# Performance work log

Measured on AMD Instinct MI355X. Metric: run time of the kernel, lower is better.

The kernel has to match this reference:

```python
import math
import jax, jax.numpy as jnp
from jax import lax
import numpy as np

NHEADS = 8
GN_GROUPS = 32
GN_EPS = 1e-5
L2_EPS = 1e-12


def conv2d(x, w, b=None, groups=1):
    # x: [B,C,H,W], w: [O, I/groups, kh, kw], stride 1, torch padding=k//2 (SAME)
    out = lax.conv_general_dilated(
        x, w, window_strides=(1, 1), padding='SAME',
        dimension_numbers=('NCHW', 'OIHW', 'NCHW'),
        feature_group_count=groups)
    if b is not None:
        out = out + b[None, :, None, None]
    return out


def group_norm(x, scale, bias, groups, eps=GN_EPS):
    B, C, H, W = x.shape
    xg = x.reshape(B, groups, C // groups, H, W)
    mu = jnp.mean(xg, axis=(2, 3, 4), keepdims=True)
    var = jnp.var(xg, axis=(2, 3, 4), keepdims=True)
    xg = (xg - mu) * lax.rsqrt(var + eps)
    x = xg.reshape(B, C, H, W)
    return x * scale[None, :, None, None] + bias[None, :, None, None]


def l2norm_ch(x):
    # F.normalize(x, dim=1): divide by channel L2 norm, clamped at eps
    n = jnp.sqrt(jnp.sum(x * x, axis=1, keepdims=True))
    return x / jnp.maximum(n, L2_EPS)


def attn_op(q, k, v, nheads, scale):
    # q,k,v: [B, C, xf, yf] real; tokens = frequency bins, features = C/nheads
    b, c, xf, yf = q.shape
    hd = c // nheads
    qh = q.reshape(b, nheads, hd, xf * yf)
    kh = k.reshape(b, nheads, hd, xf * yf)
    vh = v.reshape(b, nheads, hd, xf * yf)
    sim = jnp.einsum('bhcm,bhcn->bhmn', qh, kh) * scale
    attn = jax.nn.softmax(sim, axis=-1)
    out = jnp.einsum('bhmn,bhcn->bhcm', attn, vh)
    return out.reshape(b, c, xf, yf)


def setup_inputs() -> dict:
    key = jax.random.key(0)
    ks = jax.random.split(key, 14)
    B, H, W = 4, 48, 48
    fea = cond_c = qkv = dout = 256

    def rn(k, shape, s=0.05):
        return jax.random.normal(k, shape, dtype=jnp.float32) * s

    return {
        'x': jax.random.normal(ks[0], (B, fea, H, W), jnp.float32),
        'cond': jax.random.normal(ks[1], (B, cond_c, H, W), jnp.float32),
        'gn_w': jnp.ones((fea,), jnp.float32),
        'gn_b': jnp.zeros((fea,), jnp.float32),
        'q_dw': rn(ks[2], (fea, 1, 3, 3)),          # depthwise 3x3, groups=fea
        'q_pw_w': rn(ks[3], (qkv, fea, 1, 1)),
        'q_pw_b': jnp.zeros((qkv,), jnp.float32),
        'kv_dw': rn(ks[4], (cond_c, 1, 3, 3)),
        'kv_pw_w': rn(ks[5], (2 * qkv, cond_c, 1, 1)),
        'kv_pw_b': jnp.zeros((2 * qkv,), jnp.float32),
        'attn_out_w': rn(ks[6], (dout, qkv, 1, 1)),
        'attn_out_b': jnp.zeros((dout,), jnp.float32),
        'ffn_w1': rn(ks[7], (2 * dout, dout, 3, 3)),
        'ffn_w2': rn(ks[8], (dout, 2 * dout, 3, 3)),
        'ffn_w3': rn(ks[9], (dout, dout, 1, 1)),
        'ffn_b3': jnp.zeros((dout,), jnp.float32),
    }


def reference(x, cond, gn_w, gn_b, q_dw, q_pw_w, q_pw_b, kv_dw, kv_pw_w, kv_pw_b,
              attn_out_w, attn_out_b, ffn_w1, ffn_w2, ffn_w3, ffn_b3):
    B, C, H, W = x.shape
    qkv_dim = q_pw_w.shape[0]
    scale = 1.0 / math.sqrt(qkv_dim // NHEADS)

    xn = group_norm(x, gn_w, gn_b, GN_GROUPS)
    q = conv2d(conv2d(xn, q_dw, groups=C), q_pw_w, q_pw_b)
    kv = conv2d(conv2d(cond, kv_dw, groups=cond.shape[1]), kv_pw_w, kv_pw_b)
    k, v = jnp.split(kv, 2, axis=1)
    q, k, v = l2norm_ch(q), l2norm_ch(k), l2norm_ch(v)

    qf = jnp.fft.rfft2(q, axes=(-2, -1), norm='ortho')
    kf = jnp.fft.rfft2(k, axes=(-2, -1), norm='ortho')
    vf = jnp.fft.rfft2(v, axes=(-2, -1), norm='ortho')

    amp = attn_op(jnp.abs(qf), jnp.abs(kf), jnp.abs(vf), NHEADS, scale)
    phas = attn_op(jnp.angle(qf), jnp.angle(kf), jnp.angle(vf), NHEADS, scale)
    outc = lax.complex(amp * jnp.cos(phas), amp * jnp.sin(phas))  # torch.polar
    out = jnp.fft.irfft2(outc, s=(H, W), axes=(-2, -1), norm='ortho')

    attn_out = conv2d(out, attn_out_w, attn_out_b) + xn  # attn_res = Identity (fea_dim == dim_out)
    h1 = jax.nn.silu(conv2d(attn_out, ffn_w1))
    h2 = conv2d(h1, ffn_w2)
    ffn = conv2d(h2, ffn_w3, ffn_b3)
    # DropPath is identity in eval mode
    return ffn + attn_out
```

## Files before the change

### kernel.cpp

```cpp
#include <hip/hip_runtime.h>
#include <hip/hip_bf16.h>
#include <math.h>

constexpr int Bn = 4, Cn = 256, Hn = 48, Wn = 48, HW = 2304;
constexpr float ATT_SCALE = 0.17677669529663687f;

typedef __attribute__((ext_vector_type(8))) short bf16x8;
typedef __attribute__((ext_vector_type(4))) float f32x4;

#define MFMA16(A, B, C) __builtin_amdgcn_mfma_f32_16x16x32_bf16(A, B, C, 0, 0, 0)

__global__ void gn1_kernel(const float* __restrict__ x, float* __restrict__ part) {
  int bg = blockIdx.x >> 2, ck = blockIdx.x & 3;
  const float4* xp = (const float4*)(x + (size_t)bg * 18432 + ck * 4608);
  float s = 0.f, ss = 0.f;
  for (int i = threadIdx.x; i < 1152; i += 256) {
    float4 v = xp[i];
    s += v.x + v.y + v.z + v.w;
    ss += v.x * v.x + v.y * v.y + v.z * v.z + v.w * v.w;
  }
#pragma unroll
  for (int off = 32; off; off >>= 1) { s += __shfl_xor(s, off); ss += __shfl_xor(ss, off); }
  __shared__ float rs[4], rss[4];
  int wid = threadIdx.x >> 6;
  if ((threadIdx.x & 63) == 0) { rs[wid] = s; rss[wid] = ss; }
  __syncthreads();
  if (threadIdx.x == 0) {
    part[blockIdx.x * 2] = rs[0] + rs[1] + rs[2] + rs[3];
    part[blockIdx.x * 2 + 1] = rss[0] + rss[1] + rss[2] + rss[3];
  }
}

__global__ void gn2_kernel(const float* __restrict__ x, const float* __restrict__ part,
                           const float* __restrict__ gw, const float* __restrict__ gb,
                           float* __restrict__ y) {
  int bg = blockIdx.x >> 2, ck = blockIdx.x & 3;
  float s = part[bg * 8] + part[bg * 8 + 2] + part[bg * 8 + 4] + part[bg * 8 + 6];
  float ss = part[bg * 8 + 1] + part[bg * 8 + 3] + part[bg * 8 + 5] + part[bg * 8 + 7];
  float mean = s * (1.f / 18432.f);
  float var = ss * (1.f / 18432.f) - mean * mean;
  float inv = rsqrtf(var + 1e-5f);
  int g = bg & 31;
  const float4* xp = (const float4*)(x + (size_t)bg * 18432 + ck * 4608);
  float4* yp = (float4*)(y + (size_t)bg * 18432 + ck * 4608);
  for (int i = threadIdx.x; i < 1152; i += 256) {
    int c = (g << 3) + ((ck * 1152 + i) / 576);
    float w = gw[c] * inv, b = gb[c];
    float4 v = xp[i];
    v.x = (v.x - mean) * w + b; v.y = (v.y - mean) * w + b;
    v.z = (v.z - mean) * w + b; v.w = (v.w - mean) * w + b;
    yp[i] = v;
  }
}

__global__ void dw3x3_kernel(const float* __restrict__ in, const float* __restrict__ wd,
                             __hip_bfloat16* __restrict__ oh, __hip_bfloat16* __restrict__ ol) {
  int bc = blockIdx.x;
  int c = bc & 255;
  const float* ip = in + (size_t)bc * HW;
  const size_t ob = ((size_t)((bc >> 8) * 8 + (c >> 5)) * HW) * 32 + (c & 31);
  float w[9];
#pragma unroll
  for (int k = 0; k < 9; ++k) w[k] = wd[c * 9 + k];
  for (int p = threadIdx.x; p < HW; p += 256) {
    int yy = p / 48, xx = p - yy * 48;
    float a = 0.f;
#pragma unroll
    for (int ky = 0; ky < 3; ++ky) {
      int y2 = yy + ky - 1;
      if ((unsigned)y2 < 48u) {
#pragma unroll
        for (int kx = 0; kx < 3; ++kx) {
          int x2 = xx + kx - 1;
          if ((unsigned)x2 < 48u) a += ip[y2 * 48 + x2] * w[ky * 3 + kx];
        }
      }
    }
    __hip_bfloat16 h = __float2bfloat16(a);
    oh[ob + (size_t)p * 32] = h;
    ol[ob + (size_t)p * 32] = __float2bfloat16(a - __bfloat162float(h));
  }
}

__global__ void pwpack_kernel(const float* __restrict__ w, __hip_bfloat16* __restrict__ WH,
                              __hip_bfloat16* __restrict__ WL, int O) {
  int q = blockIdx.x * 256 + threadIdx.x;
  int o = q >> 8, c = q & 255;
  float v = w[q];
  __hip_bfloat16 h = __float2bfloat16(v);
  size_t idx = ((size_t)(c >> 5) * O + o) * 32 + (c & 31);
  WH[idx] = h;
  WL[idx] = __float2bfloat16(v - __bfloat162float(h));
}

template <bool RES>
__global__ void __launch_bounds__(256)
pw5_kernel(const __hip_bfloat16* __restrict__ XH, const __hip_bfloat16* __restrict__ XL,
           const __hip_bfloat16* __restrict__ WH, const __hip_bfloat16* __restrict__ WL,
           const float* __restrict__ bias, const float* __restrict__ res, size_t res_bs,
           float* __restrict__ out, size_t out_bs, int CO) {
  const int tid = threadIdx.x;
  const int wv = tid >> 6, lane = tid & 63, lm = lane & 15, kg = lane >> 4;
  const int px0 = blockIdx.x * 128;
  const int ob = blockIdx.y * 64;
  const int img = blockIdx.z;

  f32x4 acc[4][2];
#pragma unroll
  for (int mt = 0; mt < 4; ++mt) {
    acc[mt][0] = (f32x4){0.f, 0.f, 0.f, 0.f};
    acc[mt][1] = (f32x4){0.f, 0.f, 0.f, 0.f};
  }

  const size_t bb = (size_t)img * 589824 + (size_t)(px0 + wv * 32 + lm) * 32 + kg * 8;
#pragma unroll
  for (int ci = 0; ci < 8; ++ci) {
    const size_t bo = bb + (size_t)ci * 73728;
    bf16x8 BH0 = *(const bf16x8*)(XH + bo);
    bf16x8 BH1 = *(const bf16x8*)(XH + bo + 512);
    bf16x8 BL0 = *(const bf16x8*)(XL + bo);
    bf16x8 BL1 = *(const bf16x8*)(XL + bo + 512);
    const size_t wb = ((size_t)ci * CO + ob + lm) * 32 + kg * 8;
#pragma unroll
    for (int mt = 0; mt < 4; ++mt) {
      bf16x8 AH = *(const bf16x8*)(WH + wb + mt * 512);
      bf16x8 AL = *(const bf16x8*)(WL + wb + mt * 512);
      acc[mt][0] = MFMA16(AH, BH0, acc[mt][0]);
      acc[mt][0] = MFMA16(AH, BL0, acc[mt][0]);
      acc[mt][0] = MFMA16(AL, BH0, acc[mt][0]);
      acc[mt][1] = MFMA16(AH, BH1, acc[mt][1]);
      acc[mt][1] = MFMA16(AH, BL1, acc[mt][1]);
      acc[mt][1] = MFMA16(AL, BH1, acc[mt][1]);
    }
  }

#pragma unroll
  for (int mt = 0; mt < 4; ++mt) {
#pragma unroll
    for (int g = 0; g < 2; ++g) {
      int px = px0 + wv * 32 + g * 16 + lm;
#pragma unroll
      for (int r = 0; r < 4; ++r) {
        int o = ob + mt * 16 + kg * 4 + r;
        float v = acc[mt][g][r] + bias[o];
        if (RES) v += res[(size_t)img * res_bs + (size_t)o * HW + px];
        out[(size_t)img * out_bs + (size_t)o * HW + px] = v;
      }
    }
  }
}

__global__ void l2n_kernel(float* __restrict__ t, size_t bstride) {
  int pxl = threadIdx.x & 63;
  int cg = threadIdx.x >> 6;
  int p = blockIdx.x * 64 + pxl;
  float* q = t + (size_t)blockIdx.y * bstride + p;
  float ss = 0.f;
#pragma unroll 8
  for (int c = cg * 64; c < cg * 64 + 64; ++c) { float v = q[(size_t)c * HW]; ss += v * v; }
  __shared__ float part[4][64];
  __shared__ float sinv[64];
  part[cg][pxl] = ss;
  __syncthreads();
  if (threadIdx.x < 64) {
    float tot = part[0][pxl] + part[1][pxl] + part[2][pxl] + part[3][pxl];
    sinv[pxl] = 1.f / fmaxf(sqrtf(tot), 1e-12f);
  }
  __syncthreads();
  float inv = sinv[pxl];
#pragma unroll 8
  for (int c = cg * 64; c < cg * 64 + 64; ++c) q[(size_t)c * HW] *= inv;
}

__global__ void dftmat_kernel(__hip_bfloat16* __restrict__ mt) {
  int t = blockIdx.x * 256 + threadIdx.x;
  const float TP = 6.283185307179586f;
  if (t < 4096) {
    int up = t >> 6, w = t & 63;
    float v = 0.f;
    if (w < 48 && up < 50) {
      int u = (up < 25) ? up : up - 25;
      float ang = TP * (float)((w * u) % 48) / 48.f;
      v = ((up < 25) ? cosf(ang) : -sinf(ang)) * (1.f / 48.f);
    }
    __hip_bfloat16 h = __float2bfloat16(v);
    mt[t] = h; mt[4096 + t] = __float2bfloat16(v - __bfloat162float(h));
  } else if (t < 7168) {
    int q = t - 4096;
    int vv = q >> 6, h = q & 63;
    float c = 0.f, s = 0.f;
    if (h < 48) {
      float ang = TP * (float)((vv * h) % 48) / 48.f;
      c = cosf(ang); s = sinf(ang);
    }
    __hip_bfloat16 ch = __float2bfloat16(c);
    mt[8192 + q] = ch; mt[11264 + q] = __float2bfloat16(c - __bfloat162float(ch));
    __hip_bfloat16 sh = __float2bfloat16(s);
    mt[14336 + q] = sh; mt[17408 + q] = __float2bfloat16(s - __bfloat162float(sh));
  } else if (t < 8704) {
    int q = t - 7168;
    int w = q >> 5, u = q & 31;
    float c = 0.f, s = 0.f;
    if (u < 25) {
      float ang = TP * (float)((u * w) % 48) / 48.f;
      c = cosf(ang); s = -sinf(ang);
    }
    __hip_bfloat16 ch = __float2bfloat16(c);
    mt[20480 + q] = ch; mt[22016 + q] = __float2bfloat16(c - __bfloat162float(ch));
    __hip_bfloat16 sh = __float2bfloat16(s);
    mt[23552 + q] = sh; mt[25088 + q] = __float2bfloat16(s - __bfloat162float(sh));
  }
}

template <bool TLAY>
__global__ void __launch_bounds__(256)
rfft2_mfma(const float* __restrict__ in, size_t bstride, const __hip_bfloat16* __restrict__ mt,
           __hip_bfloat16* __restrict__ amp, __hip_bfloat16* __restrict__ pha) {
  const int bc = blockIdx.x;
  const int bi = bc >> 8, ch = bc & 255;
  const float* ip = in + (size_t)bi * bstride + (size_t)ch * HW;
  __shared__ __align__(16) __hip_bfloat16 XH[48 * 72], XL[48 * 72];
  __shared__ __align__(16) __hip_bfloat16 Yt[4][32 * 72];
  const int tid = threadIdx.x;
  const int lane = tid & 63, lm = lane & 15, kg = lane >> 4, wv = tid >> 6;

  for (int i = tid; i < 48 * 72; i += 256) {
    int r = i / 72, w = i - r * 72;
    float v = (w < 48) ? ip[r * 48 + w] : 0.f;
    __hip_bfloat16 h = __float2bfloat16(v);
    XH[i] = h;
    XL[i] = __float2bfloat16(v - __bfloat162float(h));
  }
  for (int i = tid; i < 4 * 32 * 72; i += 256) ((unsigned short*)Yt)[i] = 0;
  __syncthreads();

  {
    const __hip_bfloat16* W1TH = mt;
    const __hip_bfloat16* W1TL = mt + 4096;
    const int brow = wv * 16 + lm;
    bf16x8 BH0 = *(const bf16x8*)(W1TH + brow * 64 + kg * 8);
    bf16x8 BH1 = *(const bf16x8*)(W1TH + brow * 64 + 32 + kg * 8);
    bf16x8 BL0 = *(const bf16x8*)(W1TL + brow * 64 + kg * 8);
    bf16x8 BL1 = *(const bf16x8*)(W1TL + brow * 64 + 32 + kg * 8);
#pragma unroll
    for (int mtI = 0; mtI < 3; ++mtI) {
      f32x4 acc = {0.f, 0.f, 0.f, 0.f};
      bf16x8 AH = *(const bf16x8*)(&XH[(mtI * 16 + lm) * 72 + kg * 8]);
      bf16x8 AL = *(const bf16x8*)(&XL[(mtI * 16 + lm) * 72 + kg * 8]);
      acc = MFMA16(AH, BH0, acc); acc = MFMA16(AH, BL0, acc); acc = MFMA16(AL, BH0, acc);
      AH = *(const bf16x8*)(&XH[(mtI * 16 + lm) * 72 + 32 + kg * 8]);
      AL = *(const bf16x8*)(&XL[(mtI * 16 + lm) * 72 + 32 + kg * 8]);
      acc = MFMA16(AH, BH1, acc); acc = MFMA16(AH, BL1, acc); acc = MFMA16(AL, BH1, acc);
      if (brow < 50) {
        int aidx = (brow < 25) ? 0 : 2;
        int u = (brow < 25) ? brow : brow - 25;
#pragma unroll
        for (int r = 0; r < 4; ++r) {
          int h = mtI * 16 + kg * 4 + r;
          float v = acc[r];
          __hip_bfloat16 hh = __float2bfloat16(v);
          Yt[aidx][u * 72 + h] = hh;
          Yt[aidx + 1][u * 72 + h] = __float2bfloat16(v - __bfloat162float(hh));
        }
      }
    }
  }
  __syncthreads();

  {
    const __hip_bfloat16* M2CH = mt + 8192;
    const __hip_bfloat16* M2CL = mt + 11264;
    const __hip_bfloat16* M2SH = mt + 14336;
    const __hip_bfloat16* M2SL = mt + 17408;
    for (int t = wv; t < 6; t += 4) {
      int mtI = t >> 1, ntI = t & 1;
      f32x4 aC1 = {0.f,0.f,0.f,0.f}, aS1 = {0.f,0.f,0.f,0.f};
      f32x4 aC2 = {0.f,0.f,0.f,0.f}, aS2 = {0.f,0.f,0.f,0.f};
#pragma unroll
      for (int ks = 0; ks < 2; ++ks) {
        int arow = mtI * 16 + lm;
        int k0 = ks * 32 + kg * 8;
        bf16x8 CH = *(const bf16x8*)(M2CH + arow * 64 + k0);
        bf16x8 CL = *(const bf16x8*)(M2CL + arow * 64 + k0);
        bf16x8 SH = *(const bf16x8*)(M2SH + arow * 64 + k0);
        bf16x8 SL = *(const bf16x8*)(M2SL + arow * 64 + k0);
        int brow = ntI * 16 + lm;
        bf16x8 ReH = *(const bf16x8*)(&Yt[0][brow * 72 + k0]);
        bf16x8 ReL = *(const bf16x8*)(&Yt[1][brow * 72 + k0]);
        bf16x8 ImH = *(const bf16x8*)(&Yt[2][brow * 72 + k0]);
        bf16x8 ImL = *(const bf16x8*)(&Yt[3][brow * 72 + k0]);
        aC1 = MFMA16(CH, ReH, aC1); aC1 = MFMA16(CH, ReL, aC1); aC1 = MFMA16(CL, ReH, aC1);
        aS2 = MFMA16(SH, ImH, aS2); aS2 = MFMA16(SH, ImL, aS2); aS2 = MFMA16(SL, ImH, aS2);
        aC2 = MFMA16(CH, ImH, aC2); aC2 = MFMA16(CH, ImL, aC2); aC2 = MFMA16(CL, ImH, aC2);
        aS1 = MFMA16(SH, ReH, aS1); aS1 = MFMA16(SH, ReL, aS1); aS1 = MFMA16(SL, ReH, aS1);
      }
      int u = ntI * 16 + lm;
      if (u < 25) {
#pragma unroll
        for (int r = 0; r < 4; ++r) {
          int v = mtI * 16 + kg * 4 + r;
          float zre = aC1[r] + aS2[r];
          float zim = aC2[r] - aS1[r];
          float am = sqrtf(zre * zre + zim * zim);
          float ph = atan2f(zim, zre);
          int i = v * 25 + u;
          size_t o;
          if (TLAY) o = ((size_t)(bc >> 5) * 1200 + i) * 32 + (bc & 31);
          else      o = (size_t)bc * 1200 + i;
          amp[o] = __float2bfloat16(am);
          pha[o] = __float2bfloat16(ph);
        }
      }
    }
  }
}

__global__ void __launch_bounds__(256)
polar_irfft2_mfma(const float* __restrict__ amp, const float* __restrict__ pha,
                  const __hip_bfloat16* __restrict__ mt,
                  __hip_bfloat16* __restrict__ oh, __hip_bfloat16* __restrict__ ol) {
  const int bc = blockIdx.x;
  __shared__ __align__(16) __hip_bfloat16 Zt[4][32 * 72];
  __shared__ __align__(16) __hip_bfloat16 Yp[4][48 * 56];
  const int tid = threadIdx.x;
  const int lane = tid & 63, lm = lane & 15, kg = lane >> 4, wv = tid >> 6;

  for (int i = tid; i < 4 * 32 * 72; i += 256) ((unsigned short*)Zt)[i] = 0;
  for (int i = tid; i < 4 * 48 * 56; i += 256) ((unsigned short*)Yp)[i] = 0;
  __syncthreads();
  for (int i = tid; i < 1200; i += 256) {
    int v = i / 25, u = i - v * 25;
    float a = amp[(size_t)bc * 1200 + i];
    float p = pha[(size_t)bc * 1200 + i];
    float sc = (u == 0 || u == 24) ? (1.f / 48.f) : (2.f / 48.f);
    float zre = a * cosf(p) * sc;
    float zim = a * sinf(p) * sc;
    __hip_bfloat16 h0 = __float2bfloat16(zre);
    Zt[0][u * 72 + v] = h0;
    Zt[1][u * 72 + v] = __float2bfloat16(zre - __bfloat162float(h0));
    __hip_bfloat16 h1 = __float2bfloat16(zim);
    Zt[2][u * 72 + v] = h1;
    Zt[3][u * 72 + v] = __float2bfloat16(zim - __bfloat162float(h1));
  }
  __syncthreads();

  {
    const __hip_bfloat16* M2CH = mt + 8192;
    const __hip_bfloat16* M2CL = mt + 11264;
    const __hip_bfloat16* M2SH = mt + 14336;
    const __hip_bfloat16* M2SL = mt + 17408;
    for (int t = wv; t < 6; t += 4) {
      int mtI = t >> 1, ntI = t & 1;
      f32x4 aC1 = {0.f,0.f,0.f,0.f}, aS1 = {0.f,0.f,0.f,0.f};
      f32x4 aC2 = {0.f,0.f,0.f,0.f}, aS2 = {0.f,0.f,0.f,0.f};
#pragma unroll
      for (int ks = 0; ks < 2; ++ks) {
        int arow = mtI * 16 + lm;
        int k0 = ks * 32 + kg * 8;
        bf16x8 CH = *(const bf16x8*)(M2CH + arow * 64 + k0);
        bf16x8 CL = *(const bf16x8*)(M2CL + arow * 64 + k0);
        bf16x8 SH = *(const bf16x8*)(M2SH + arow * 64 + k0);
        bf16x8 SL = *(const bf16x8*)(M2SL + arow * 64 + k0);
        int brow = ntI * 16 + lm;
        bf16x8 ReH = *(const bf16x8*)(&Zt[0][brow * 72 + k0]);
        bf16x8 ReL = *(const bf16x8*)(&Zt[1][brow * 72 + k0]);
        bf16x8 ImH = *(const bf16x8*)(&Zt[2][brow * 72 + k0]);
        bf16x8 ImL = *(const bf16x8*)(&Zt[3][brow * 72 + k0]);
        aC1 = MFMA16(CH, ReH, aC1); aC1 = MFMA16(CH, ReL, aC1); aC1 = MFMA16(CL, ReH, aC1);
        aS2 = MFMA16(SH, ImH, aS2); aS2 = MFMA16(SH, ImL, aS2); aS2 = MFMA16(SL, ImH, aS2);
        aC2 = MFMA16(CH, ImH, aC2); aC2 = MFMA16(CH, ImL, aC2); aC2 = MFMA16(CL, ImH, aC2);
        aS1 = MFMA16(SH, ReH, aS1); aS1 = MFMA16(SH, ReL, aS1); aS1 = MFMA16(SL, ReH, aS1);
      }
      int u = ntI * 16 + lm;
      if (u < 25) {
#pragma unroll
        for (int r = 0; r < 4; ++r) {
          int h = mtI * 16 + kg * 4 + r;
          float yre = aC1[r] - aS2[r];
          float yim = aS1[r] + aC2[r];
          __hip_bfloat16 h0 = __float2bfloat16(yre);
          Yp[0][h * 56 + u] = h0;
          Yp[1][h * 56 + u] = __float2bfloat16(yre - __bfloat162float(h0));
          __hip_bfloat16 h1 = __float2bfloat16(yim);
          Yp[2][h * 56 + u] = h1;
          Yp[3][h * 56 + u] = __float2bfloat16(yim - __bfloat162float(h1));
        }
      }
    }
  }
  __syncthreads();

  {
    const __hip_bfloat16* W3CH = mt + 20480;
    const __hip_bfloat16* W3CL = mt + 22016;
    const __hip_bfloat16* W3SH = mt + 23552;
    const __hip_bfloat16* W3SL = mt + 25088;
    const int cch = bc & 255;
    const size_t obase = ((size_t)((bc >> 8) * 8 + (cch >> 5)) * HW) * 32 + (cch & 31);
    for (int t = wv; t < 9; t += 4) {
      int mtI = t / 3, ntI = t - (t / 3) * 3;
      f32x4 acc = {0.f, 0.f, 0.f, 0.f};
      int k0 = kg * 8;
      bf16x8 AH = *(const bf16x8*)(&Yp[0][(mtI * 16 + lm) * 56 + k0]);
      bf16x8 AL = *(const bf16x8*)(&Yp[1][(mtI * 16 + lm) * 56 + k0]);
      bf16x8 IH = *(const bf16x8*)(&Yp[2][(mtI * 16 + lm) * 56 + k0]);
      bf16x8 IL = *(const bf16x8*)(&Yp[3][(mtI * 16 + lm) * 56 + k0]);
      int brow = ntI * 16 + lm;
      bf16x8 CH = *(const bf16x8*)(W3CH + brow * 32 + k0);
      bf16x8 CL = *(const bf16x8*)(W3CL + brow * 32 + k0);
      bf16x8 SH = *(const bf16x8*)(W3SH + brow * 32 + k0);
      bf16x8 SL = *(const bf16x8*)(W3SL + brow * 32 + k0);
      acc = MFMA16(AH, CH, acc); acc = MFMA16(AH, CL, acc); acc = MFMA16(AL, CH, acc);
      acc = MFMA16(IH, SH, acc); acc = MFMA16(IH, SL, acc); acc = MFMA16(IL, SH, acc);
#pragma unroll
      for (int r = 0; r < 4; ++r) {
        int h = mtI * 16 + kg * 4 + r;
        int p = h * 48 + brow;
        float v = acc[r];
        __hip_bfloat16 hh = __float2bfloat16(v);
        oh[obase + (size_t)p * 32] = hh;
        ol[obase + (size_t)p * 32] = __float2bfloat16(v - __bfloat162float(hh));
      }
    }
  }
}

__global__ void __launch_bounds__(64)
attn_mfma2x(const __hip_bfloat16* __restrict__ Qb, const __hip_bfloat16* __restrict__ Kb,
            const __hip_bfloat16* __restrict__ Vb, float* __restrict__ Ob) {
  const int lin = blockIdx.x;
  const int xcd = lin & 7;
  const int idx = lin >> 3;
  const int pr = xcd * 8 + idx / 75;
  const int m0 = (idx % 75) * 16;
  const int z = pr >> 5;
  const int bh = pr & 31;
  const __hip_bfloat16* Qt = Qb + (size_t)z * 1228800;
  const __hip_bfloat16* Kt = Kb + (size_t)z * 1228800;
  const __hip_bfloat16* Vc = Vb + (size_t)z * 1228800;
  float* Om = Ob + (size_t)z * 1228800;
  const int lane = threadIdx.x;
  const int lm = lane & 15, kg = lane >> 4;
  __shared__ unsigned short Pl[16][40];
  __shared__ float fl[16];
  __shared__ float linv[16];
  const __hip_bfloat16* Qp = Qt + ((size_t)bh * 1200 + m0) * 32;
  const __hip_bfloat16* Kp = Kt + (size_t)bh * 38400;
  const __hip_bfloat16* Vp = Vc + (size_t)bh * 38400;
  const bf16x8 qf = *(const bf16x8*)(Qp + lm * 32 + kg * 8);
  const float Cs = ATT_SCALE * 1.44269504f;

  f32x4 acc0 = {0.f, 0.f, 0.f, 0.f}, acc1 = {0.f, 0.f, 0.f, 0.f};
  float psum = 0.f, mreg = -3.0e38f;

  for (int g = 0; g < 38; ++g) {
    const int n0 = g * 32;
    const bool t1ok = (g < 37);
    bf16x8 kf0 = *(const bf16x8*)(Kp + (size_t)(n0 + lm) * 32 + kg * 8);
    f32x4 d0 = {0.f, 0.f, 0.f, 0.f};
    d0 = MFMA16(kf0, qf, d0);
    f32x4 d1 = {0.f, 0.f, 0.f, 0.f};
    if (t1ok) {
      bf16x8 kf1 = *(const bf16x8*)(Kp + (size_t)(n0 + 16 + lm) * 32 + kg * 8);
      d1 = MFMA16(kf1, qf, d1);
    }
    float tm = fmaxf(fmaxf(d0[0], d0[1]), fmaxf(d0[2], d0[3]));
    if (t1ok) tm = fmaxf(tm, fmaxf(fmaxf(d1[0], d1[1]), fmaxf(d1[2], d1[3])));
    tm = fmaxf(tm, __shfl_xor(tm, 16));
    tm = fmaxf(tm, __shfl_xor(tm, 32));
    float nm = fmaxf(mreg, tm);
    float ff = exp2f((mreg - nm) * Cs);
    mreg = nm;
    if (kg == 0) fl[lm] = ff;
    const float mb = nm * Cs;
    float p0 = exp2f(d0[0] * Cs - mb), p1 = exp2f(d0[1] * Cs - mb);
    float p2 = exp2f(d0[2] * Cs - mb), p3 = exp2f(d0[3] * Cs - mb);
    float ps = p0 + p1 + p2 + p3;
    ushort4 pk0, pk1;
    pk0.x = __builtin_bit_cast(unsigned short, __float2bfloat16(p0));
    pk0.y = __builtin_bit_cast(unsigned short, __float2bfloat16(p1));
    pk0.z = __builtin_bit_cast(unsigned short, __float2bfloat16(p2));
    pk0.w = __builtin_bit_cast(unsigned short, __float2bfloat16(p3));
    if (t1ok) {
      float q0 = exp2f(d1[0] * Cs - mb), q1 = exp2f(d1[1] * Cs - mb);
      float q2 = exp2f(d1[2] * Cs - mb), q3 = exp2f(d1[3] * Cs - mb);
      ps += q0 + q1 + q2 + q3;
      pk1.x = __builtin_bit_cast(unsigned short, __float2bfloat16(q0));
      pk1.y = __builtin_bit_cast(unsigned short, __float2bfloat16(q1));
      pk1.z = __builtin_bit_cast(unsigned short, __float2bfloat16(q2));
      pk1.w = __builtin_bit_cast(unsigned short, __float2bfloat16(q3));
    } else {
      pk1.x = pk1.y = pk1.z = pk1.w = 0;
    }
    psum = psum * ff + ps;
    *(ushort4*)(&Pl[lm][kg * 4]) = pk0;
    *(ushort4*)(&Pl[lm][16 + kg * 4]) = pk1;
    float4 f4 = *(const float4*)(&fl[kg * 4]);
    acc0[0] *= f4.x; acc0[1] *= f4.y; acc0[2] *= f4.z; acc0[3] *= f4.w;
    acc1[0] *= f4.x; acc1[1] *= f4.y; acc1[2] *= f4.z; acc1[3] *= f4.w;
    bf16x8 pa = *(const bf16x8*)(&Pl[lm][kg * 8]);
    bf16x8 v0 = *(const bf16x8*)(Vp + (size_t)lm * 1200 + n0 + kg * 8);
    bf16x8 v1 = *(const bf16x8*)(Vp + (size_t)(16 + lm) * 1200 + n0 + kg * 8);
    acc0 = MFMA16(pa, v0, acc0);
    acc1 = MFMA16(pa, v1, acc1);
  }
  psum += __shfl_xor(psum, 16);
  psum += __shfl_xor(psum, 32);
  if (kg == 0) linv[lm] = 1.f / psum;
  __syncthreads();
#pragma unroll
  for (int r = 0; r < 4; ++r) {
    int m = m0 + kg * 4 + r;
    float li = linv[kg * 4 + r];
    Om[(size_t)bh * 38400 + (size_t)lm * 1200 + m] = acc0[r] * li;
    Om[(size_t)bh * 38400 + (size_t)(16 + lm) * 1200 + m] = acc1[r] * li;
  }
}

__global__ void packx_kernel(const float* __restrict__ in, __hip_bfloat16* __restrict__ xp) {
  int y = blockIdx.x;
  int b = blockIdx.y;
  int c = threadIdx.x;
  const float* ip = in + ((size_t)(b * 256 + c) * 48 + y) * 48;
  __hip_bfloat16* op = xp + ((size_t)(b * 8 + (c >> 5)) * 2500 + (size_t)(y + 1) * 50 + 1) * 32 + (c & 31);
  for (int x = 0; x < 48; ++x) op[x * 32] = __float2bfloat16(ip[x]);
}

template <int CIN>
__global__ void packw_kernel(const float* __restrict__ w, __hip_bfloat16* __restrict__ wp, int O) {
  int t = blockIdx.x * 256 + threadIdx.x;
  int o = t / CIN, c = t - o * CIN;
  if (o >= O) return;
  constexpr int NC = CIN / 32;
#pragma unroll
  for (int tap = 0; tap < 9; ++tap)
    wp[(((size_t)tap * NC + (c >> 5)) * O + o) * 32 + (c & 31)] = __float2bfloat16(w[(size_t)t * 9 + tap]);
}

__global__ void addpack_kernel(const float* __restrict__ a, const float* __restrict__ b,
                               __hip_bfloat16* __restrict__ oh, __hip_bfloat16* __restrict__ ol) {
  int i = blockIdx.x * 256 + threadIdx.x;
  float4 x = ((const float4*)a)[i];
  float4 y = ((const float4*)b)[i];
  x.x += y.x; x.y += y.y; x.z += y.z; x.w += y.w;
  int e = i * 4;
  int img = e / 589824, rem = e - img * 589824;
  int c = rem / 2304, px = rem - c * 2304;
  size_t ob = ((size_t)(img * 8 + (c >> 5)) * HW) * 32 + (c & 31);
  float vv[4] = {x.x, x.y, x.z, x.w};
#pragma unroll
  for (int j = 0; j < 4; ++j) {
    __hip_bfloat16 h = __float2bfloat16(vv[j]);
    oh[ob + (size_t)(px + j) * 32] = h;
    ol[ob + (size_t)(px + j) * 32] = __float2bfloat16(vv[j] - __bfloat162float(h));
  }
}

template <int CIN, int CO, bool TO_PAD, int KS>
__global__ void __launch_bounds__(256)
mfconv3x3(const __hip_bfloat16* __restrict__ Xp, const __hip_bfloat16* __restrict__ Wp,
          __hip_bfloat16* __restrict__ Op, float* __restrict__ Of) {
  constexpr int NC = CIN / 32;
  constexpr int KC = NC / KS;
  constexpr int MT = CO / 32;
  const int q = gridDim.x >> 3;
  const int swz = (blockIdx.x & 7) * q + (blockIdx.x >> 3);
  const int mt = swz % MT;
  const int ks = (swz / MT) % KS;
  const int rq = swz / (MT * KS);
  const int img = rq / 12;
  const int y0b = (rq % 12) * 4;
  const int tid = threadIdx.x;
  const int wv = tid >> 6;
  const int y = y0b + wv;
  const int lane = tid & 63;
  const int lm = lane & 15, kg = lane >> 4;
  const int o0 = mt * 32;
  const int ci0 = ks * KC;

  __shared__ __hip_bfloat16 Als[9216];
  __shared__ __hip_bfloat16 Bls[9600];

  f32x4 acc[2][3];
#pragma unroll
  for (int f = 0; f < 2; ++f)
#pragma unroll
    for (int g = 0; g < 3; ++g) acc[f][g] = (f32x4){0.f, 0.f, 0.f, 0.f};

  for (int ci = 0; ci < KC; ++ci) {
    const int cic = ci0 + ci;
    const size_t wst = ((size_t)cic * CO + o0) * 32;
    const size_t bst = ((size_t)(img * NC + cic) * 2500 + (size_t)y0b * 50) * 32;
    __syncthreads();
    for (int c = tid; c < 2352; c += 256) {
      if (c < 1152) {
        int tap = c >> 7, rem = c & 127;
        float4 v = *(const float4*)(Wp + wst + (size_t)tap * (NC * CO * 32) + rem * 8);
        *(float4*)(&Als[c * 8]) = v;
      } else {
        int c2 = c - 1152;
        float4 v = *(const float4*)(Xp + bst + (size_t)c2 * 8);
        *(float4*)(&Bls[c2 * 8]) = v;
      }
    }
    __syncthreads();
#pragma unroll
    for (int tap = 0; tap < 9; ++tap) {
      const int dy = tap / 3 - 1, dx = tap - (tap / 3) * 3 - 1;
      bf16x8 A0 = *(const bf16x8*)(&Als[tap * 1024 + lm * 32 + kg * 8]);
      bf16x8 A1 = *(const bf16x8*)(&Als[tap * 1024 + 512 + lm * 32 + kg * 8]);
      const int bbase = ((wv + 1 + dy) * 50 + 1 + dx + lm) * 32 + kg * 8;
      bf16x8 B0 = *(const bf16x8*)(&Bls[bbase]);
      bf16x8 B1 = *(const bf16x8*)(&Bls[bbase + 512]);
      bf16x8 B2 = *(const bf16x8*)(&Bls[bbase + 1024]);
      acc[0][0] = MFMA16(A0, B0, acc[0][0]);
      acc[0][1] = MFMA16(A0, B1, acc[0][1]);
      acc[0][2] = MFMA16(A0, B2, acc[0][2]);
      acc[1][0] = MFMA16(A1, B0, acc[1][0]);
      acc[1][1] = MFMA16(A1, B1, acc[1][1]);
      acc[1][2] = MFMA16(A1, B2, acc[1][2]);
    }
  }

  if (TO_PAD) {
    const int cio = o0 >> 5;
#pragma unroll
    for (int f = 0; f < 2; ++f) {
      const int cc = f * 16 + kg * 4;
#pragma unroll
      for (int g = 0; g < 3; ++g) {
        int x = g * 16 + lm;
        ushort4 st;
        float v0 = acc[f][g][0], v1 = acc[f][g][1], v2 = acc[f][g][2], v3 = acc[f][g][3];
        v0 = v0 / (1.f + __expf(-v0)); v1 = v1 / (1.f + __expf(-v1));
        v2 = v2 / (1.f + __expf(-v2)); v3 = v3 / (1.f + __expf(-v3));
        st.x = __builtin_bit_cast(unsigned short, __float2bfloat16(v0));
        st.y = __builtin_bit_cast(unsigned short, __float2bfloat16(v1));
        st.z = __builtin_bit_cast(unsigned short, __float2bfloat16(v2));
        st.w = __builtin_bit_cast(unsigned short, __float2bfloat16(v3));
        *(ushort4*)(Op + (((size_t)(img * (CO / 32) + cio) * 2500 + (size_t)(y + 1) * 50 + (x + 1)) * 32 + cc)) = st;
      }
    }
  } else {
    float* Ofp = Of + (size_t)ks * 4 * CO * HW;
#pragma unroll
    for (int f = 0; f < 2; ++f)
#pragma unroll
      for (int g = 0; g < 3; ++g) {
        int x = g * 16 + lm;
#pragma unroll
        for (int r = 0; r < 4; ++r) {
          int o = o0 + f * 16 + kg * 4 + r;
          Ofp[((size_t)img * CO + o) * HW + y * 48 + x] = acc[f][g][r];
        }
      }
  }
}

extern "C" void kernel_launch(void* const* d_in, const int* in_sizes, int n_in,
                              void* d_out, int out_size, void* d_ws, size_t ws_size,
                              hipStream_t stream) {
  (void)in_sizes; (void)n_in; (void)out_size; (void)ws_size;
  const float* x      = (const float*)d_in[0];
  const float* cond   = (const float*)d_in[1];
  const float* gn_w   = (const float*)d_in[2];
  const float* gn_b   = (const float*)d_in[3];
  const float* q_dw   = (const float*)d_in[4];
  const float* q_pw_w = (const float*)d_in[5];
  const float* q_pw_b = (const float*)d_in[6];
  const float* kv_dw  = (const float*)d_in[7];
  const float* kv_pw_w= (const float*)d_in[8];
  const float* kv_pw_b= (const float*)d_in[9];
  const float* ao_w   = (const float*)d_in[10];
  const float* ao_b   = (const float*)d_in[11];
  const float* w1     = (const float*)d_in[12];
  const float* w2     = (const float*)d_in[13];
  const float* w3     = (const float*)d_in[14];
  const float* b3     = (const float*)d_in[15];
  float* ws = (float*)d_ws;
  float* Yo = (float*)d_out;

  const size_t U = 2359296;
  const size_t Hf = 1228800;
  const size_t CS = 589824;
  const size_t CS2 = 1179648;

  float* XN  = ws;
  __hip_bfloat16* DWH = (__hip_bfloat16*)(ws + U);
  __hip_bfloat16* DWL = DWH + 2359296;
  float* Qb  = ws + 2 * U;
  float* KV  = ws + 3 * U;
  __hip_bfloat16* AQT = (__hip_bfloat16*)(ws + 5 * U);
  __hip_bfloat16* PQT = AQT + 1228800;
  __hip_bfloat16* AKT = AQT + 2 * 1228800;
  __hip_bfloat16* PKT = AQT + 3 * 1228800;
  __hip_bfloat16* AVc = AQT + 4 * 1228800;
  __hip_bfloat16* PVc = AQT + 5 * 1228800;
  float* AO  = ws + 5 * U + 3 * Hf;
  float* PO  = AO + Hf;
  __hip_bfloat16* OUTH = (__hip_bfloat16*)(ws + U);
  __hip_bfloat16* OUTL = OUTH + 2359296;
  float* ATT = ws + 5 * U;
  __hip_bfloat16* Xp1 = (__hip_bfloat16*)(ws + U);
  __hip_bfloat16* Xp2 = (__hip_bfloat16*)(ws + 2 * U);
  __hip_bfloat16* Wp1 = (__hip_bfloat16*)(ws + 2 * U + 2600000);
  __hip_bfloat16* Wp2 = (__hip_bfloat16*)(ws + 2 * U + 3200000);
  float* H2  = ws;
  float* H2b = ws + U;
  __hip_bfloat16* H2H = (__hip_bfloat16*)(ws + 5 * U + 3 * Hf);
  __hip_bfloat16* H2L = H2H + 2359296;
  __hip_bfloat16* BW = (__hip_bfloat16*)(ws + 5 * U + 5 * Hf);
  __hip_bfloat16* QWH = BW,            * QWL = BW + 65536;
  __hip_bfloat16* KWH = BW + 131072,   * KWL = BW + 262144;
  __hip_bfloat16* AWH = BW + 393216,   * AWL = BW + 458752;
  __hip_bfloat16* W3H = BW + 524288,   * W3L = BW + 589824;
  __hip_bfloat16* MT  = BW + 655360;
  float* GNP = ws + 5 * U + 5 * Hf + 341000;

  pwpack_kernel<<<256, 256, 0, stream>>>(q_pw_w, QWH, QWL, 256);
  pwpack_kernel<<<512, 256, 0, stream>>>(kv_pw_w, KWH, KWL, 512);
  pwpack_kernel<<<256, 256, 0, stream>>>(ao_w, AWH, AWL, 256);
  pwpack_kernel<<<256, 256, 0, stream>>>(w3, W3H, W3L, 256);
  dftmat_kernel<<<34, 256, 0, stream>>>(MT);
  gn1_kernel<<<512, 256, 0, stream>>>(x, GNP);
  gn2_kernel<<<512, 256, 0, stream>>>(x, GNP, gn_w, gn_b, XN);
  dw3x3_kernel<<<1024, 256, 0, stream>>>(XN, q_dw, DWH, DWL);
  pw5_kernel<false><<<dim3(18, 4, 4), 256, 0, stream>>>(DWH, DWL, QWH, QWL, q_pw_b, nullptr, 0, Qb, CS, 256);
  dw3x3_kernel<<<1024, 256, 0, stream>>>(cond, kv_dw, DWH, DWL);
  pw5_kernel<false><<<dim3(18, 8, 4), 256, 0, stream>>>(DWH, DWL, KWH, KWL, kv_pw_b, nullptr, 0, KV, CS2, 512);
  l2n_kernel<<<dim3(36, 4), 256, 0, stream>>>(Qb, CS);
  l2n_kernel<<<dim3(36, 4), 256, 0, stream>>>(KV, CS2);
  l2n_kernel<<<dim3(36, 4), 256, 0, stream>>>(KV + CS, CS2);
  rfft2_mfma<true ><<<1024, 256, 0, stream>>>(Qb, CS, MT, AQT, PQT);
  rfft2_mfma<true ><<<1024, 256, 0, stream>>>(KV, CS2, MT, AKT, PKT);
  rfft2_mfma<false><<<1024, 256, 0, stream>>>(KV + CS, CS2, MT, AVc, PVc);
  attn_mfma2x<<<4800, 64, 0, stream>>>(AQT, AKT, AVc, AO);
  polar_irfft2_mfma<<<1024, 256, 0, stream>>>(AO, PO, MT, OUTH, OUTL);
  pw5_kernel<true><<<dim3(18, 4, 4), 256, 0, stream>>>(OUTH, OUTL, AWH, AWL, ao_b, XN, CS, ATT, CS, 256);
  hipMemsetAsync(Xp1, 0, 2560000 * sizeof(__hip_bfloat16), stream);
  hipMemsetAsync(Xp2, 0, 5120000 * sizeof(__hip_bfloat16), stream);
  packx_kernel<<<dim3(48, 4), 256, 0, stream>>>(ATT, Xp1);
  packw_kernel<256><<<512, 256, 0, stream>>>(w1, Wp1, 512);
  packw_kernel<512><<<512, 256, 0, stream>>>(w2, Wp2, 256);
  mfconv3x3<256, 512, true, 1><<<768, 256, 0, stream>>>(Xp1, Wp1, Xp2, nullptr);
  mfconv3x3<512, 256, false, 2><<<768, 256, 0, stream>>>(Xp2, Wp2, nullptr, H2);
  addpack_kernel<<<2304, 256, 0, stream>>>(H2, H2b, H2H, H2L);
  pw5_kernel<true><<<dim3(18, 4, 4), 256, 0, stream>>>(H2H, H2L, W3H, W3L, b3, ATT, CS, Yo, CS, 256);
}
```

Before: 484.7 us.

## Widen attention key tiles, skip redundant rescales, register-prefetch conv input slabs

The frequency-domain attention kernel now processes 64 keys per iteration instead of 32. It also skips the online-softmax rescale of the accumulators and row sums when no row maximum grows, using a wave ballot to decide. The 3x3 conv kernel no longer stages weights in LDS; it reads them directly from global memory per tap. It also double-buffers the input slab through registers so the next channel chunk's load overlaps the current MFMAs. Together these cut loop overhead, exp and rescale work, and LDS traffic, at the cost of more registers and uncached global weight reads.

```diff
diff --git a/kernel.cpp b/kernel.cpp
--- a/kernel.cpp
+++ b/kernel.cpp
@@ -426,8 +426,8 @@
 }
 
 __global__ void __launch_bounds__(64)
-attn_mfma2x(const __hip_bfloat16* __restrict__ Qb, const __hip_bfloat16* __restrict__ Kb,
-            const __hip_bfloat16* __restrict__ Vb, float* __restrict__ Ob) {
+attn_mfma5(const __hip_bfloat16* __restrict__ Qb, const __hip_bfloat16* __restrict__ Kb,
+           const __hip_bfloat16* __restrict__ Vb, float* __restrict__ Ob) {
   const int lin = blockIdx.x;
   const int xcd = lin & 7;
   const int idx = lin >> 3;
@@ -441,7 +441,7 @@
   float* Om = Ob + (size_t)z * 1228800;
   const int lane = threadIdx.x;
   const int lm = lane & 15, kg = lane >> 4;
-  __shared__ unsigned short Pl[16][40];
+  __shared__ unsigned short Pl[2][16][40];
   __shared__ float fl[16];
   __shared__ float linv[16];
   const __hip_bfloat16* Qp = Qt + ((size_t)bh * 1200 + m0) * 32;
@@ -453,56 +453,86 @@
   f32x4 acc0 = {0.f, 0.f, 0.f, 0.f}, acc1 = {0.f, 0.f, 0.f, 0.f};
   float psum = 0.f, mreg = -3.0e38f;
 
-  for (int g = 0; g < 38; ++g) {
-    const int n0 = g * 32;
-    const bool t1ok = (g < 37);
+  for (int G = 0; G < 19; ++G) {
+    const int n0 = G * 64;
+    const bool s3ok = (G < 18);
     bf16x8 kf0 = *(const bf16x8*)(Kp + (size_t)(n0 + lm) * 32 + kg * 8);
-    f32x4 d0 = {0.f, 0.f, 0.f, 0.f};
-    d0 = MFMA16(kf0, qf, d0);
-    f32x4 d1 = {0.f, 0.f, 0.f, 0.f};
-    if (t1ok) {
-      bf16x8 kf1 = *(const bf16x8*)(Kp + (size_t)(n0 + 16 + lm) * 32 + kg * 8);
-      d1 = MFMA16(kf1, qf, d1);
-    }
-    float tm = fmaxf(fmaxf(d0[0], d0[1]), fmaxf(d0[2], d0[3]));
-    if (t1ok) tm = fmaxf(tm, fmaxf(fmaxf(d1[0], d1[1]), fmaxf(d1[2], d1[3])));
+    bf16x8 kf1 = *(const bf16x8*)(Kp + (size_t)(n0 + 16 + lm) * 32 + kg * 8);
+    bf16x8 kf2 = *(const bf16x8*)(Kp + (size_t)(n0 + 32 + lm) * 32 + kg * 8);
+    f32x4 d0 = {0.f, 0.f, 0.f, 0.f}; d0 = MFMA16(kf0, qf, d0);
+    f32x4 d1 = {0.f, 0.f, 0.f, 0.f}; d1 = MFMA16(kf1, qf, d1);
+    f32x4 d2 = {0.f, 0.f, 0.f, 0.f}; d2 = MFMA16(kf2, qf, d2);
+    f32x4 d3 = {0.f, 0.f, 0.f, 0.f};
+    if (s3ok) {
+      bf16x8 kf3 = *(const bf16x8*)(Kp + (size_t)(n0 + 48 + lm) * 32 + kg * 8);
+      d3 = MFMA16(kf3, qf, d3);
+    }
+    float tm = fmaxf(fmaxf(fmaxf(d0[0], d0[1]), fmaxf(d0[2], d0[3])),
+                     fmaxf(fmaxf(d1[0], d1[1]), fmaxf(d1[2], d1[3])));
+    tm = fmaxf(tm, fmaxf(fmaxf(d2[0], d2[1]), fmaxf(d2[2], d2[3])));
+    if (s3ok) tm = fmaxf(tm, fmaxf(fmaxf(d3[0], d3[1]), fmaxf(d3[2], d3[3])));
     tm = fmaxf(tm, __shfl_xor(tm, 16));
     tm = fmaxf(tm, __shfl_xor(tm, 32));
-    float nm = fmaxf(mreg, tm);
-    float ff = exp2f((mreg - nm) * Cs);
-    mreg = nm;
-    if (kg == 0) fl[lm] = ff;
-    const float mb = nm * Cs;
+    const bool grow = (__ballot(tm > mreg) != 0ull);
+    if (grow) {
+      float nm = fmaxf(mreg, tm);
+      float ff = exp2f((mreg - nm) * Cs);
+      mreg = nm;
+      if (kg == 0) fl[lm] = ff;
+      psum *= ff;
+    }
+    const float mb = mreg * Cs;
     float p0 = exp2f(d0[0] * Cs - mb), p1 = exp2f(d0[1] * Cs - mb);
     float p2 = exp2f(d0[2] * Cs - mb), p3 = exp2f(d0[3] * Cs - mb);
-    float ps = p0 + p1 + p2 + p3;
-    ushort4 pk0, pk1;
-    pk0.x = __builtin_bit_cast(unsigned short, __float2bfloat16(p0));
-    pk0.y = __builtin_bit_cast(unsigned short, __float2bfloat16(p1));
-    pk0.z = __builtin_bit_cast(unsigned short, __float2bfloat16(p2));
-    pk0.w = __builtin_bit_cast(unsigned short, __float2bfloat16(p3));
-    if (t1ok) {
-      float q0 = exp2f(d1[0] * Cs - mb), q1 = exp2f(d1[1] * Cs - mb);
-      float q2 = exp2f(d1[2] * Cs - mb), q3 = exp2f(d1[3] * Cs - mb);
-      ps += q0 + q1 + q2 + q3;
-      pk1.x = __builtin_bit_cast(unsigned short, __float2bfloat16(q0));
-      pk1.y = __builtin_bit_cast(unsigned short, __float2bfloat16(q1));
-      pk1.z = __builtin_bit_cast(unsigned short, __float2bfloat16(q2));
-      pk1.w = __builtin_bit_cast(unsigned short, __float2bfloat16(q3));
+    float p4 = exp2f(d1[0] * Cs - mb), p5 = exp2f(d1[1] * Cs - mb);
+    float p6 = exp2f(d1[2] * Cs - mb), p7 = exp2f(d1[3] * Cs - mb);
+    float p8 = exp2f(d2[0] * Cs - mb), p9 = exp2f(d2[1] * Cs - mb);
+    float pa_ = exp2f(d2[2] * Cs - mb), pb_ = exp2f(d2[3] * Cs - mb);
+    float ps = p0 + p1 + p2 + p3 + p4 + p5 + p6 + p7 + p8 + p9 + pa_ + pb_;
+    ushort4 w0, w1, w2, w3;
+    w0.x = __builtin_bit_cast(unsigned short, __float2bfloat16(p0));
+    w0.y = __builtin_bit_cast(unsigned short, __float2bfloat16(p1));
+    w0.z = __builtin_bit_cast(unsigned short, __float2bfloat16(p2));
+    w0.w = __builtin_bit_cast(unsigned short, __float2bfloat16(p3));
+    w1.x = __builtin_bit_cast(unsigned short, __float2bfloat16(p4));
+    w1.y = __builtin_bit_cast(unsigned short, __float2bfloat16(p5));
+    w1.z = __builtin_bit_cast(unsigned short, __float2bfloat16(p6));
+    w1.w = __builtin_bit_cast(unsigned short, __float2bfloat16(p7));
+    w2.x = __builtin_bit_cast(unsigned short, __float2bfloat16(p8));
+    w2.y = __builtin_bit_cast(unsigned short, __float2bfloat16(p9));
+    w2.z = __builtin_bit_cast(unsigned short, __float2bfloat16(pa_));
+    w2.w = __builtin_bit_cast(unsigned short, __float2bfloat16(pb_));
+    if (s3ok) {
+      float pc_ = exp2f(d3[0] * Cs - mb), pd_ = exp2f(d3[1] * Cs - mb);
+      float pe_ = exp2f(d3[2] * Cs - mb), pf_ = exp2f(d3[3] * Cs - mb);
+      ps += pc_ + pd_ + pe_ + pf_;
+      w3.x = __builtin_bit_cast(unsigned short, __float2bfloat16(pc_));
+      w3.y = __builtin_bit_cast(unsigned short, __float2bfloat16(pd_));
+      w3.z = __builtin_bit_cast(unsigned short, __float2bfloat16(pe_));
+      w3.w = __builtin_bit_cast(unsigned short, __float2bfloat16(pf_));
     } else {
-      pk1.x = pk1.y = pk1.z = pk1.w = 0;
-    }
-    psum = psum * ff + ps;
-    *(ushort4*)(&Pl[lm][kg * 4]) = pk0;
-    *(ushort4*)(&Pl[lm][16 + kg * 4]) = pk1;
-    float4 f4 = *(const float4*)(&fl[kg * 4]);
-    acc0[0] *= f4.x; acc0[1] *= f4.y; acc0[2] *= f4.z; acc0[3] *= f4.w;
-    acc1[0] *= f4.x; acc1[1] *= f4.y; acc1[2] *= f4.z; acc1[3] *= f4.w;
-    bf16x8 pa = *(const bf16x8*)(&Pl[lm][kg * 8]);
-    bf16x8 v0 = *(const bf16x8*)(Vp + (size_t)lm * 1200 + n0 + kg * 8);
-    bf16x8 v1 = *(const bf16x8*)(Vp + (size_t)(16 + lm) * 1200 + n0 + kg * 8);
-    acc0 = MFMA16(pa, v0, acc0);
-    acc1 = MFMA16(pa, v1, acc1);
+      w3.x = w3.y = w3.z = w3.w = 0;
+    }
+    psum += ps;
+    *(ushort4*)(&Pl[0][lm][kg * 4]) = w0;
+    *(ushort4*)(&Pl[0][lm][16 + kg * 4]) = w1;
+    *(ushort4*)(&Pl[1][lm][kg * 4]) = w2;
+    *(ushort4*)(&Pl[1][lm][16 + kg * 4]) = w3;
+    if (grow) {
+      float4 f4 = *(const float4*)(&fl[kg * 4]);
+      acc0[0] *= f4.x; acc0[1] *= f4.y; acc0[2] *= f4.z; acc0[3] *= f4.w;
+      acc1[0] *= f4.x; acc1[1] *= f4.y; acc1[2] *= f4.z; acc1[3] *= f4.w;
+    }
+    bf16x8 pa0 = *(const bf16x8*)(&Pl[0][lm][kg * 8]);
+    bf16x8 pa1 = *(const bf16x8*)(&Pl[1][lm][kg * 8]);
+    bf16x8 v00 = *(const bf16x8*)(Vp + (size_t)lm * 1200 + n0 + kg * 8);
+    bf16x8 v01 = *(const bf16x8*)(Vp + (size_t)(16 + lm) * 1200 + n0 + kg * 8);
+    bf16x8 v10 = *(const bf16x8*)(Vp + (size_t)lm * 1200 + n0 + 32 + kg * 8);
+    bf16x8 v11 = *(const bf16x8*)(Vp + (size_t)(16 + lm) * 1200 + n0 + 32 + kg * 8);
+    acc0 = MFMA16(pa0, v00, acc0);
+    acc1 = MFMA16(pa0, v01, acc1);
+    acc0 = MFMA16(pa1, v10, acc0);
+    acc1 = MFMA16(pa1, v11, acc1);
   }
   psum += __shfl_xor(psum, 16);
   psum += __shfl_xor(psum, 32);
@@ -578,8 +608,7 @@
   const int o0 = mt * 32;
   const int ci0 = ks * KC;
 
-  __shared__ __hip_bfloat16 Als[9216];
-  __shared__ __hip_bfloat16 Bls[9600];
+  __shared__ __align__(16) __hip_bfloat16 Bls[9600];
 
   f32x4 acc[2][3];
 #pragma unroll
@@ -587,28 +616,38 @@
 #pragma unroll
     for (int g = 0; g < 3; ++g) acc[f][g] = (f32x4){0.f, 0.f, 0.f, 0.f};
 
+  const float4* X4 = (const float4*)Xp;
+  const size_t slab0 = ((size_t)(img * NC + ci0) * 2500 + (size_t)y0b * 50) * 4;
+
+  float4 s0, s1, s2, s3, s4;
+  {
+    size_t b4 = slab0;
+    s0 = X4[b4 + tid]; s1 = X4[b4 + tid + 256];
+    s2 = X4[b4 + tid + 512]; s3 = X4[b4 + tid + 768];
+    if (tid < 176) s4 = X4[b4 + tid + 1024];
+  }
+
   for (int ci = 0; ci < KC; ++ci) {
-    const int cic = ci0 + ci;
-    const size_t wst = ((size_t)cic * CO + o0) * 32;
-    const size_t bst = ((size_t)(img * NC + cic) * 2500 + (size_t)y0b * 50) * 32;
     __syncthreads();
-    for (int c = tid; c < 2352; c += 256) {
-      if (c < 1152) {
-        int tap = c >> 7, rem = c & 127;
-        float4 v = *(const float4*)(Wp + wst + (size_t)tap * (NC * CO * 32) + rem * 8);
-        *(float4*)(&Als[c * 8]) = v;
-      } else {
-        int c2 = c - 1152;
-        float4 v = *(const float4*)(Xp + bst + (size_t)c2 * 8);
-        *(float4*)(&Bls[c2 * 8]) = v;
-      }
+    {
+      float4* B4 = (float4*)Bls;
+      B4[tid] = s0; B4[tid + 256] = s1; B4[tid + 512] = s2; B4[tid + 768] = s3;
+      if (tid < 176) B4[tid + 1024] = s4;
     }
     __syncthreads();
+    if (ci + 1 < KC) {
+      size_t b4 = slab0 + (size_t)(ci + 1) * 10000;
+      s0 = X4[b4 + tid]; s1 = X4[b4 + tid + 256];
+      s2 = X4[b4 + tid + 512]; s3 = X4[b4 + tid + 768];
+      if (tid < 176) s4 = X4[b4 + tid + 1024];
+    }
+    const __hip_bfloat16* wbase = Wp + ((size_t)(ci0 + ci) * CO + o0 + lm) * 32 + kg * 8;
 #pragma unroll
     for (int tap = 0; tap < 9; ++tap) {
       const int dy = tap / 3 - 1, dx = tap - (tap / 3) * 3 - 1;
-      bf16x8 A0 = *(const bf16x8*)(&Als[tap * 1024 + lm * 32 + kg * 8]);
-      bf16x8 A1 = *(const bf16x8*)(&Als[tap * 1024 + 512 + lm * 32 + kg * 8]);
+      const __hip_bfloat16* wp_ = wbase + (size_t)tap * (NC * CO * 32);
+      bf16x8 A0 = *(const bf16x8*)(wp_);
+      bf16x8 A1 = *(const bf16x8*)(wp_ + 512);
       const int bbase = ((wv + 1 + dy) * 50 + 1 + dx + lm) * 32 + kg * 8;
       bf16x8 B0 = *(const bf16x8*)(&Bls[bbase]);
       bf16x8 B1 = *(const bf16x8*)(&Bls[bbase + 512]);
@@ -734,7 +773,7 @@
   rfft2_mfma<true ><<<1024, 256, 0, stream>>>(Qb, CS, MT, AQT, PQT);
   rfft2_mfma<true ><<<1024, 256, 0, stream>>>(KV, CS2, MT, AKT, PKT);
   rfft2_mfma<false><<<1024, 256, 0, stream>>>(KV + CS, CS2, MT, AVc, PVc);
-  attn_mfma2x<<<4800, 64, 0, stream>>>(AQT, AKT, AVc, AO);
+  attn_mfma5<<<4800, 64, 0, stream>>>(AQT, AKT, AVc, AO);
   polar_irfft2_mfma<<<1024, 256, 0, stream>>>(AO, PO, MT, OUTH, OUTL);
   pw5_kernel<true><<<dim3(18, 4, 4), 256, 0, stream>>>(OUTH, OUTL, AWH, AWL, ao_b, XN, CS, ATT, CS, 256);
   hipMemsetAsync(Xp1, 0, 2560000 * sizeof(__hip_bfloat16), stream);
```

Measured after the change: 503.3 us. 3.8% more time.
